# Kernel optimization log

Measured on AMD Instinct MI355X. Metric: run time of the kernel, lower is better.

## Reference

```python
import jax, jax.numpy as jnp
import numpy as np

N, E = 50000, 500000
IN_C, HID, OUT_C, HEADS, NL = 128, 16, 16, 8, 4
EPS = 1e-5
NEG_SLOPE = 0.2


def _gatv2(x, src, dst, Wl, Wr, att, bias, concat):
    # GATv2Conv (PyG semantics, eval mode): lin_l on source, lin_r on target,
    # e = a . LeakyReLU(xl[src] + xr[dst]); segment softmax over dst; scatter-sum.
    n = x.shape[0]
    H, C = att.shape
    xl = (x @ Wl).reshape(n, H, C)
    xr = (x @ Wr).reshape(n, H, C)
    e = jax.nn.leaky_relu(xl[src] + xr[dst], NEG_SLOPE)          # [E', H, C]
    logit = jnp.einsum('ehc,hc->eh', e, att)                      # [E', H]
    mx = jax.lax.stop_gradient(jax.ops.segment_max(logit, dst, num_segments=n))
    a = jnp.exp(logit - mx[dst])
    denom = jax.ops.segment_sum(a, dst, num_segments=n)
    alpha = a / denom[dst]                                        # [E', H]
    out = jax.ops.segment_sum(xl[src] * alpha[..., None], dst, num_segments=n)
    out = out.reshape(n, H * C) if concat else out.mean(axis=1)
    return out + bias


def _bn_eval(x, g, b, m, v):
    return (x - m) * jax.lax.rsqrt(v + EPS) * g + b


def setup_inputs() -> dict:
    key = jax.random.key(0)
    ks = jax.random.split(key, 32)
    d = {}
    d['x'] = jax.random.normal(ks[0], (N, IN_C), dtype=jnp.float32)
    d['edge_index'] = jax.random.randint(ks[1], (2, E), 0, N, dtype=jnp.int64)
    HC = HID * HEADS  # 128
    dims_in = [IN_C, HC, HC, HC]
    dims_h = [HEADS, HEADS, HEADS, 1]
    dims_c = [HID, HID, HID, OUT_C]
    ki = 2
    for i in range(NL):
        fan = dims_in[i]
        s = 1.0 / np.sqrt(fan)
        d[f'W{i}l'] = jax.random.uniform(ks[ki], (fan, dims_h[i] * dims_c[i]), minval=-s, maxval=s, dtype=jnp.float32); ki += 1
        d[f'W{i}r'] = jax.random.uniform(ks[ki], (fan, dims_h[i] * dims_c[i]), minval=-s, maxval=s, dtype=jnp.float32); ki += 1
        d[f'a{i}'] = jax.random.normal(ks[ki], (dims_h[i], dims_c[i]), dtype=jnp.float32) * 0.1; ki += 1
        out_dim = dims_h[i] * dims_c[i] if i < NL - 1 else dims_c[i]
        d[f'b{i}'] = jnp.zeros((out_dim,), dtype=jnp.float32)
    for i in range(NL - 1):
        d[f'g{i}'] = jnp.ones((HC,), dtype=jnp.float32) + 0.1 * jax.random.normal(ks[ki], (HC,), dtype=jnp.float32); ki += 1
        d[f'be{i}'] = 0.1 * jax.random.normal(ks[ki], (HC,), dtype=jnp.float32); ki += 1
        d[f'm{i}'] = 0.1 * jax.random.normal(ks[ki], (HC,), dtype=jnp.float32); ki += 1
        d[f'v{i}'] = jnp.ones((HC,), dtype=jnp.float32)
    return d


def reference(x, edge_index, W0l, W0r, a0, b0, W1l, W1r, a1, b1, W2l, W2r, a2, b2, W3l, W3r, a3, b3, g0, be0, m0, v0, g1, be1, m1, v1, g2, be2, m2, v2):
    n = x.shape[0]
    loop = jnp.arange(n, dtype=edge_index.dtype)
    src = jnp.concatenate([edge_index[0], loop])  # add_self_loops=True (PyG default)
    dst = jnp.concatenate([edge_index[1], loop])
    Ws = [(W0l, W0r, a0, b0), (W1l, W1r, a1, b1), (W2l, W2r, a2, b2), (W3l, W3r, a3, b3)]
    bns = [(g0, be0, m0, v0), (g1, be1, m1, v1), (g2, be2, m2, v2)]
    h = x
    for i in range(NL):
        Wl, Wr, att, bias = Ws[i]
        h = _gatv2(h, src, dst, Wl, Wr, att, bias, concat=(i < NL - 1))
        if i < NL - 1:
            g, b, m, v = bns[i]
            h = jax.nn.elu(_bn_eval(h, g, b, m, v))
    return h
```

## Files before the change

kernel.cpp:

```cpp
#include <hip/hip_runtime.h>
#include <hip/hip_fp16.h>
#include <math.h>

static constexpr float BN_EPS = 1e-5f;
static constexpr float NEG = 0.2f;

typedef float f32x4 __attribute__((ext_vector_type(4)));
typedef _Float16 h16x2 __attribute__((ext_vector_type(2)));
typedef _Float16 h16x8 __attribute__((ext_vector_type(8)));


__global__ void hist_kernel(const int* __restrict__ ei, int E, int n, int* __restrict__ cnt) {
    int e = blockIdx.x * blockDim.x + threadIdx.x;
    int ET = E + n;
    if (e >= ET) return;
    int d = (e < E) ? ei[E + e] : (e - E);
    atomicAdd(&cnt[d], 1);
}

__global__ void scan_block(const int* __restrict__ cnt, int* __restrict__ rowptr,
                           int* __restrict__ bsums, int n) {
    __shared__ int s[1024];
    int i = blockIdx.x * 1024 + threadIdx.x;
    int vv = (i < n) ? cnt[i] : 0;
    s[threadIdx.x] = vv;
    __syncthreads();
    for (int d = 1; d < 1024; d <<= 1) {
        int t = (threadIdx.x >= d) ? s[threadIdx.x - d] : 0;
        __syncthreads();
        s[threadIdx.x] += t;
        __syncthreads();
    }
    if (i < n) rowptr[i + 1] = s[threadIdx.x];
    if (threadIdx.x == 1023) bsums[blockIdx.x] = s[1023];
}

__global__ void scan_bsums(int* __restrict__ bsums, int nb) {
    int L = threadIdx.x;
    int v = (L < nb) ? bsums[L] : 0;
    for (int d = 1; d < 64; d <<= 1) {
        int t = __shfl_up(v, d);
        if (L >= d) v += t;
    }
    int ex = __shfl_up(v, 1);
    if (L == 0) ex = 0;
    if (L < nb) bsums[L] = ex;
}

__global__ void scan_add(int* __restrict__ rowptr, const int* __restrict__ bsums, int n) {
    int i = blockIdx.x * 1024 + threadIdx.x;
    if (i < n) rowptr[i + 1] += bsums[blockIdx.x];
    if (i == 0) rowptr[0] = 0;
}

__global__ void scatter_kernel(const int* __restrict__ ei, int E, int n,
                               const int* __restrict__ rowptr, int* __restrict__ fill,
                               int* __restrict__ col) {
    int e = blockIdx.x * blockDim.x + threadIdx.x;
    int ET = E + n;
    if (e >= ET) return;
    int s, d;
    if (e < E) { s = ei[e]; d = ei[E + e]; } else { s = e - E; d = s; }
    int pos = atomicAdd(&fill[d], 1);
    col[rowptr[d] + pos] = s;
}


__global__ void convert_h(const float* __restrict__ x, __half* __restrict__ xh, int total4) {
    int i = blockIdx.x * blockDim.x + threadIdx.x;
    if (i >= total4) return;
    float4 v = *(const float4*)&x[(size_t)i * 4];
    __half h[4] = {__float2half(v.x), __float2half(v.y), __float2half(v.z), __float2half(v.w)};
    *(ushort4*)&xh[(size_t)i * 4] = make_ushort4(
        __half_as_ushort(h[0]), __half_as_ushort(h[1]),
        __half_as_ushort(h[2]), __half_as_ushort(h[3]));
}


__global__ void pack_w(const float* __restrict__ Wl, const float* __restrict__ Wr,
                       __half* __restrict__ packed, int M, int NTT) {
    int tile = blockIdx.x;
    int NT = NTT >> 1;
    int gnt = tile % NTT;
    int kt = tile / NTT;
    int l = threadIdx.x;
    const float* W = (gnt < NT) ? Wl : Wr;
    int col = (gnt % NT) * 16 + (l & 15);
    int krow = kt * 32 + ((l >> 4) << 3);
    size_t base = (size_t)tile * 512 + (size_t)l * 8;
#pragma unroll
    for (int j = 0; j < 8; j++)
        packed[base + j] = __float2half(W[(size_t)(krow + j) * M + col]);
}


__global__ __launch_bounds__(256) void gemm_h_big(
    const __half* __restrict__ xh, const __half* __restrict__ packed,
    __half* __restrict__ Y1, __half* __restrict__ Y2, int n) {
    __shared__ _Float16 sA[64 * 136];
    const int t = threadIdx.x;
    const int row0 = blockIdx.x * 64;

    for (int c = t; c < 1024; c += 256) {
        int row = c >> 4;
        int off = (c & 15) * 8;
        int gr = row0 + row;
        if (gr >= n) gr = n - 1;
        *(h16x8*)&sA[row * 136 + off] = *(const h16x8*)&xh[(size_t)gr * 128 + off];
    }
    __syncthreads();

    const int lane = t & 63;
    const int s = t >> 6;
    const int lr = lane & 15;
    const int kq = (lane >> 4) * 8;

    h16x8 af[4][4];
#pragma unroll
    for (int rt = 0; rt < 4; rt++)
#pragma unroll
        for (int kt = 0; kt < 4; kt++)
            af[rt][kt] = *(const h16x8*)&sA[(rt * 16 + lr) * 136 + kt * 32 + kq];

    f32x4 acc[4][4];
#pragma unroll
    for (int a = 0; a < 4; a++)
#pragma unroll
        for (int b = 0; b < 4; b++) acc[a][b] = (f32x4){0.f, 0.f, 0.f, 0.f};

#pragma unroll
    for (int kt = 0; kt < 4; kt++) {
#pragma unroll
        for (int ntl = 0; ntl < 4; ntl++) {
            int nt = s * 4 + ntl;
            h16x8 b = *(const h16x8*)&packed[((size_t)(kt * 16 + nt)) * 512 + lane * 8];
#pragma unroll
            for (int rt = 0; rt < 4; rt++)
                acc[ntl][rt] = __builtin_amdgcn_mfma_f32_16x16x32_f16(af[rt][kt], b, acc[ntl][rt], 0, 0, 0);
        }
    }

    __half* Y = (s < 2) ? Y1 : Y2;
    const int colh = (s & 1) * 64;
    const int rq = (lane >> 4) * 4;
#pragma unroll
    for (int ntl = 0; ntl < 4; ntl++) {
        int col = colh + ntl * 16 + lr;
#pragma unroll
        for (int rt = 0; rt < 4; rt++) {
#pragma unroll
            for (int g = 0; g < 4; g++) {
                int row = row0 + rt * 16 + rq + g;
                if (row < n) Y[(size_t)row * 128 + col] = __float2half(acc[ntl][rt][g]);
            }
        }
    }
}


__global__ __launch_bounds__(256) void gemm_h_small(
    const __half* __restrict__ xh, const __half* __restrict__ packed,
    float* __restrict__ Y1, float* __restrict__ Y2, int n) {
    int lane = threadIdx.x & 63;
    int wv = blockIdx.x * 4 + (threadIdx.x >> 6);
    int row0 = wv * 16;
    if (row0 >= n) return;
    int r = row0 + (lane & 15);
    if (r >= n) r = n - 1;
    int kq = (lane >> 4) * 8;

    h16x8 af[4];
#pragma unroll
    for (int kt = 0; kt < 4; kt++)
        af[kt] = *(const h16x8*)&xh[(size_t)r * 128 + kt * 32 + kq];

    f32x4 acc[2];
    acc[0] = (f32x4){0.f, 0.f, 0.f, 0.f};
    acc[1] = (f32x4){0.f, 0.f, 0.f, 0.f};

#pragma unroll
    for (int kt = 0; kt < 4; kt++) {
#pragma unroll
        for (int nt = 0; nt < 2; nt++) {
            h16x8 b = *(const h16x8*)&packed[((size_t)(kt * 2 + nt)) * 512 + lane * 8];
            acc[nt] = __builtin_amdgcn_mfma_f32_16x16x32_f16(af[kt], b, acc[nt], 0, 0, 0);
        }
    }

    int colb = lane & 15;
    int rbase = row0 + (lane >> 4) * 4;
#pragma unroll
    for (int nt = 0; nt < 2; nt++) {
        float* Y = (nt == 0) ? Y1 : Y2;
#pragma unroll
        for (int g = 0; g < 4; g++) {
            int row = rbase + g;
            if (row < n) Y[(size_t)row * 16 + colb] = acc[nt][g];
        }
    }
}


__device__ __forceinline__ float dot4_h(h16x2 l01, h16x2 l23,
                                        h16x2 a01, h16x2 a23) {
#if __has_builtin(__builtin_amdgcn_fdot2)
    float part = __builtin_amdgcn_fdot2(l01, a01, 0.f, false);
    return __builtin_amdgcn_fdot2(l23, a23, part, false);
#else
    return fmaf((float)l01.x, (float)a01.x, fmaf((float)l01.y, (float)a01.y,
           fmaf((float)l23.x, (float)a23.x, (float)l23.y * (float)a23.y)));
#endif
}

__global__ __launch_bounds__(256) void agg_h(
    const __half* __restrict__ xl, const __half* __restrict__ xr,
    const int* __restrict__ rowptr, const int* __restrict__ col,
    const float* __restrict__ att, const float* __restrict__ bias,
    const float* __restrict__ g, const float* __restrict__ be,
    const float* __restrict__ bm, const float* __restrict__ bv,
    __half* __restrict__ oh, int n) {
    int v = (blockIdx.x * blockDim.x + threadIdx.x) >> 6;
    if (v >= n) return;
    int lane = threadIdx.x & 63;
    int half = lane >> 5;
    int L = lane & 31;
    int ch = 4 * L;

    float2 rraw = *(const float2*)&xr[(size_t)v * 128 + ch];
    h16x2 rx01 = *(h16x2*)&rraw.x;
    h16x2 rx23 = *(h16x2*)&rraw.y;
    float4 av = *(const float4*)&att[ch];
    h16x2 a01 = {(_Float16)av.x, (_Float16)av.y};
    h16x2 a23 = {(_Float16)av.z, (_Float16)av.w};
    const h16x2 neg2 = {(_Float16)NEG, (_Float16)NEG};

    int beg = rowptr[v];
    int end = rowptr[v + 1];

    float lrun = 0.f;
    float4 acc = make_float4(0.f, 0.f, 0.f, 0.f);

    auto proc = [&](float2 raw, bool ok) {
        h16x2 h01 = *(h16x2*)&raw.x;
        h16x2 h23 = *(h16x2*)&raw.y;
        h16x2 s01 = h01 + rx01;
        h16x2 s23 = h23 + rx23;
        h16x2 l01 = __builtin_elementwise_max(s01, s01 * neg2);
        h16x2 l23 = __builtin_elementwise_max(s23, s23 * neg2);
        float part = dot4_h(l01, l23, a01, a23);
        part += __shfl_xor(part, 1);
        part += __shfl_xor(part, 2);
        float p = ok ? __expf(part) : 0.f;
        lrun += p;
        acc.x = fmaf(p, (float)h01.x, acc.x);
        acc.y = fmaf(p, (float)h01.y, acc.y);
        acc.z = fmaf(p, (float)h23.x, acc.z);
        acc.w = fmaf(p, (float)h23.y, acc.w);
    };

    int e = beg;
    for (; e + 8 <= end; e += 8) {
        float2 r[4];
#pragma unroll
        for (int j = 0; j < 4; j++) {
            int u = col[e + 2 * j + half];
            r[j] = *(const float2*)&xl[((size_t)u << 7) + ch];
        }
#pragma unroll
        for (int j = 0; j < 4; j++) proc(r[j], true);
    }
    for (; e < end; e += 4) {
        float2 r[2];
        bool ok[2];
#pragma unroll
        for (int j = 0; j < 2; j++) {
            int idx = e + 2 * j + half;
            ok[j] = (idx < end);
            r[j] = make_float2(0.f, 0.f);
            if (ok[j]) {
                int u = col[idx];
                r[j] = *(const float2*)&xl[((size_t)u << 7) + ch];
            }
        }
#pragma unroll
        for (int j = 0; j < 2; j++) proc(r[j], ok[j]);
    }

    lrun += __shfl_xor(lrun, 32);
    acc.x += __shfl_xor(acc.x, 32);
    acc.y += __shfl_xor(acc.y, 32);
    acc.z += __shfl_xor(acc.z, 32);
    acc.w += __shfl_xor(acc.w, 32);

    if (half == 0) {
        float inv = 1.0f / lrun;
        float4 b4 = *(const float4*)&bias[ch];
        float o[4] = {fmaf(acc.x, inv, b4.x), fmaf(acc.y, inv, b4.y),
                      fmaf(acc.z, inv, b4.z), fmaf(acc.w, inv, b4.w)};
        float4 m4 = *(const float4*)&bm[ch];
        float4 v4 = *(const float4*)&bv[ch];
        float4 g4 = *(const float4*)&g[ch];
        float4 e4 = *(const float4*)&be[ch];
        float ms[4] = {m4.x, m4.y, m4.z, m4.w};
        float vs[4] = {v4.x, v4.y, v4.z, v4.w};
        float gs[4] = {g4.x, g4.y, g4.z, g4.w};
        float es[4] = {e4.x, e4.y, e4.z, e4.w};
        unsigned short h[4];
#pragma unroll
        for (int j = 0; j < 4; j++) {
            o[j] = (o[j] - ms[j]) * rsqrtf(vs[j] + BN_EPS) * gs[j] + es[j];
            o[j] = o[j] > 0.f ? o[j] : expm1f(o[j]);
            h[j] = __half_as_ushort(__float2half(o[j]));
        }
        *(ushort4*)&oh[(size_t)v * 128 + ch] = make_ushort4(h[0], h[1], h[2], h[3]);
    }
}


__global__ __launch_bounds__(256) void agg_f(
    const float* __restrict__ xl, const float* __restrict__ xr,
    const int* __restrict__ rowptr, const int* __restrict__ col,
    const float* __restrict__ att, const float* __restrict__ bias,
    float* __restrict__ out, int n) {
    int v = (blockIdx.x * blockDim.x + threadIdx.x) >> 6;
    if (v >= n) return;
    int lane = threadIdx.x & 63;
    int slot = lane >> 2;
    int L = lane & 3;
    int ch = 4 * L;

    float4 xrv = *(const float4*)&xr[(size_t)v * 16 + ch];
    float4 av = *(const float4*)&att[ch];
    int beg = rowptr[v];
    int end = rowptr[v + 1];

    float lrun = 0.f;
    float4 acc = make_float4(0.f, 0.f, 0.f, 0.f);

    for (int eb = beg; eb < end; eb += 16) {
        int idx = eb + slot;
        bool ok = (idx < end);
        float4 xv = make_float4(0.f, 0.f, 0.f, 0.f);
        if (ok) {
            int u = col[idx];
            xv = *(const float4*)&xl[((size_t)u << 4) + ch];
        }
        float s0 = xv.x + xrv.x; s0 = s0 > 0.f ? s0 : NEG * s0;
        float s1 = xv.y + xrv.y; s1 = s1 > 0.f ? s1 : NEG * s1;
        float s2 = xv.z + xrv.z; s2 = s2 > 0.f ? s2 : NEG * s2;
        float s3 = xv.w + xrv.w; s3 = s3 > 0.f ? s3 : NEG * s3;
        float part = fmaf(s0, av.x, fmaf(s1, av.y, fmaf(s2, av.z, s3 * av.w)));
        part += __shfl_xor(part, 1);
        part += __shfl_xor(part, 2);
        float p = ok ? __expf(part) : 0.f;
        lrun += p;
        acc.x = fmaf(p, xv.x, acc.x);
        acc.y = fmaf(p, xv.y, acc.y);
        acc.z = fmaf(p, xv.z, acc.z);
        acc.w = fmaf(p, xv.w, acc.w);
    }

#pragma unroll
    for (int d = 4; d < 64; d <<= 1) {
        lrun += __shfl_xor(lrun, d);
        acc.x += __shfl_xor(acc.x, d);
        acc.y += __shfl_xor(acc.y, d);
        acc.z += __shfl_xor(acc.z, d);
        acc.w += __shfl_xor(acc.w, d);
    }

    if (slot == 0) {
        float inv = 1.0f / lrun;
        float4 b4 = *(const float4*)&bias[ch];
        *(float4*)&out[(size_t)v * 16 + ch] =
            make_float4(fmaf(acc.x, inv, b4.x), fmaf(acc.y, inv, b4.y),
                        fmaf(acc.z, inv, b4.z), fmaf(acc.w, inv, b4.w));
    }
}


extern "C" void kernel_launch(void* const* d_in, const int* in_sizes, int n_in,
                              void* d_out, int out_size, void* d_ws, size_t ws_size,
                              hipStream_t stream) {
    const float* x = (const float*)d_in[0];
    const int* ei = (const int*)d_in[1];
    const float* Wl[4] = {(const float*)d_in[2], (const float*)d_in[6],
                          (const float*)d_in[10], (const float*)d_in[14]};
    const float* Wr[4] = {(const float*)d_in[3], (const float*)d_in[7],
                          (const float*)d_in[11], (const float*)d_in[15]};
    const float* att[4] = {(const float*)d_in[4], (const float*)d_in[8],
                           (const float*)d_in[12], (const float*)d_in[16]};
    const float* bias[4] = {(const float*)d_in[5], (const float*)d_in[9],
                            (const float*)d_in[13], (const float*)d_in[17]};
    const float* g[3] = {(const float*)d_in[18], (const float*)d_in[22], (const float*)d_in[26]};
    const float* be[3] = {(const float*)d_in[19], (const float*)d_in[23], (const float*)d_in[27]};
    const float* bm[3] = {(const float*)d_in[20], (const float*)d_in[24], (const float*)d_in[28]};
    const float* bv[3] = {(const float*)d_in[21], (const float*)d_in[25], (const float*)d_in[29]};

    const int n = in_sizes[0] / 128;
    const int E = in_sizes[1] / 2;
    const int ET = E + n;

    char* p = (char*)d_ws;
    __half* xh = (__half*)p;           p += (size_t)n * 128 * 2;
    __half* xlh = (__half*)p;          p += (size_t)n * 128 * 2;
    __half* xrh = (__half*)p;          p += (size_t)n * 128 * 2;
    float* xl3 = (float*)p;            p += (size_t)n * 16 * 4;
    float* xr3 = (float*)p;            p += (size_t)n * 16 * 4;
    int* rowptr = (int*)p;            p += (size_t)(n + 1) * 4;
    int* cnt = (int*)p;               p += (size_t)n * 4;
    int* fill = (int*)p;              p += (size_t)n * 4;
    int* col = (int*)p;               p += (size_t)ET * 4;
    int* bsums = (int*)p;             p += 256;
    __half* pk[4];
    for (int i = 0; i < 3; i++) { pk[i] = (__half*)p; p += 4 * 16 * 512 * 2; }
    pk[3] = (__half*)p;               p += 4 * 2 * 512 * 2;

    (void)hipMemsetAsync(cnt, 0, (size_t)n * 4, stream);
    (void)hipMemsetAsync(fill, 0, (size_t)n * 4, stream);

    const int tb = 256;
    hist_kernel<<<(ET + tb - 1) / tb, tb, 0, stream>>>(ei, E, n, cnt);
    int nb = (n + 1023) / 1024;
    scan_block<<<nb, 1024, 0, stream>>>(cnt, rowptr, bsums, n);
    scan_bsums<<<1, 64, 0, stream>>>(bsums, nb);
    scan_add<<<nb, 1024, 0, stream>>>(rowptr, bsums, n);
    scatter_kernel<<<(ET + tb - 1) / tb, tb, 0, stream>>>(ei, E, n, rowptr, fill, col);

    convert_h<<<(n * 32 + 255) / 256, 256, 0, stream>>>(x, xh, n * 32);
    for (int i = 0; i < 3; i++)
        pack_w<<<4 * 16, 64, 0, stream>>>(Wl[i], Wr[i], pk[i], 128, 16);
    pack_w<<<4 * 2, 64, 0, stream>>>(Wl[3], Wr[3], pk[3], 16, 2);

    const int gb64 = (n + 63) / 64;
    const int gemmBlocksSmall = ((n + 15) / 16 + 3) / 4;
    const int aggBlocks = (n + 3) / 4;

    for (int i = 0; i < 3; i++) {
        gemm_h_big<<<gb64, 256, 0, stream>>>(xh, pk[i], xlh, xrh, n);
        agg_h<<<aggBlocks, 256, 0, stream>>>(
            xlh, xrh, rowptr, col, att[i], bias[i], g[i], be[i], bm[i], bv[i],
            xh, n);
    }
    gemm_h_small<<<gemmBlocksSmall, 256, 0, stream>>>(xh, pk[3], xl3, xr3, n);
    agg_f<<<aggBlocks, 256, 0, stream>>>(
        xl3, xr3, rowptr, col, att[3], bias[3], (float*)d_out, n);
}
```

Measured before the change: 385.4 us.

## Process four edges per wavefront with 16-byte loads in fp16 aggregation

New measurement: 415.8 us. +7.9%, slower.

```diff
diff --git a/kernel.cpp b/kernel.cpp
--- a/kernel.cpp
+++ b/kernel.cpp
@@ -201,14 +201,11 @@
 }
 
 
-__device__ __forceinline__ float dot4_h(h16x2 l01, h16x2 l23,
-                                        h16x2 a01, h16x2 a23) {
+__device__ __forceinline__ float fdot2w(h16x2 x, h16x2 y, float init) {
 #if __has_builtin(__builtin_amdgcn_fdot2)
-    float part = __builtin_amdgcn_fdot2(l01, a01, 0.f, false);
-    return __builtin_amdgcn_fdot2(l23, a23, part, false);
+    return __builtin_amdgcn_fdot2(x, y, init, false);
 #else
-    return fmaf((float)l01.x, (float)a01.x, fmaf((float)l01.y, (float)a01.y,
-           fmaf((float)l23.x, (float)a23.x, (float)l23.y * (float)a23.y)));
+    return fmaf((float)x.x, (float)y.x, fmaf((float)x.y, (float)y.y, init));
 #endif
 }
 
@@ -222,97 +219,85 @@
     int v = (blockIdx.x * blockDim.x + threadIdx.x) >> 6;
     if (v >= n) return;
     int lane = threadIdx.x & 63;
-    int half = lane >> 5;
-    int L = lane & 31;
-    int ch = 4 * L;
-
-    float2 rraw = *(const float2*)&xr[(size_t)v * 128 + ch];
-    h16x2 rx01 = *(h16x2*)&rraw.x;
-    h16x2 rx23 = *(h16x2*)&rraw.y;
-    float4 av = *(const float4*)&att[ch];
-    h16x2 a01 = {(_Float16)av.x, (_Float16)av.y};
-    h16x2 a23 = {(_Float16)av.z, (_Float16)av.w};
-    const h16x2 neg2 = {(_Float16)NEG, (_Float16)NEG};
+    int slot = lane >> 4;
+    int L = lane & 15;
+    int ch = 8 * L;
+
+    h16x8 rx = *(const h16x8*)&xr[(size_t)v * 128 + ch];
+    h16x2 a01, a23, a45, a67;
+    {
+        float4 f0 = *(const float4*)&att[ch];
+        float4 f1 = *(const float4*)&att[ch + 4];
+        a01 = (h16x2){(_Float16)f0.x, (_Float16)f0.y};
+        a23 = (h16x2){(_Float16)f0.z, (_Float16)f0.w};
+        a45 = (h16x2){(_Float16)f1.x, (_Float16)f1.y};
+        a67 = (h16x2){(_Float16)f1.z, (_Float16)f1.w};
+    }
+    const h16x8 negv = {(_Float16)NEG, (_Float16)NEG, (_Float16)NEG, (_Float16)NEG,
+                        (_Float16)NEG, (_Float16)NEG, (_Float16)NEG, (_Float16)NEG};
 
     int beg = rowptr[v];
     int end = rowptr[v + 1];
 
     float lrun = 0.f;
-    float4 acc = make_float4(0.f, 0.f, 0.f, 0.f);
-
-    auto proc = [&](float2 raw, bool ok) {
-        h16x2 h01 = *(h16x2*)&raw.x;
-        h16x2 h23 = *(h16x2*)&raw.y;
-        h16x2 s01 = h01 + rx01;
-        h16x2 s23 = h23 + rx23;
-        h16x2 l01 = __builtin_elementwise_max(s01, s01 * neg2);
-        h16x2 l23 = __builtin_elementwise_max(s23, s23 * neg2);
-        float part = dot4_h(l01, l23, a01, a23);
+    float acc[8];
+#pragma unroll
+    for (int k = 0; k < 8; k++) acc[k] = 0.f;
+
+    for (int eb = beg; eb < end; eb += 4) {
+        int idx = eb + slot;
+        bool ok = (idx < end);
+        h16x8 x = (h16x8){0, 0, 0, 0, 0, 0, 0, 0};
+        if (ok) {
+            int u = col[idx];
+            x = *(const h16x8*)&xl[((size_t)u << 7) + ch];
+        }
+        h16x8 s = x + rx;
+        h16x8 l = __builtin_elementwise_max(s, s * negv);
+        float part = fdot2w((h16x2){l[0], l[1]}, a01, 0.f);
+        part = fdot2w((h16x2){l[2], l[3]}, a23, part);
+        part = fdot2w((h16x2){l[4], l[5]}, a45, part);
+        part = fdot2w((h16x2){l[6], l[7]}, a67, part);
         part += __shfl_xor(part, 1);
-        part += __shfl_xor(part, 2);
         float p = ok ? __expf(part) : 0.f;
         lrun += p;
-        acc.x = fmaf(p, (float)h01.x, acc.x);
-        acc.y = fmaf(p, (float)h01.y, acc.y);
-        acc.z = fmaf(p, (float)h23.x, acc.z);
-        acc.w = fmaf(p, (float)h23.y, acc.w);
-    };
-
-    int e = beg;
-    for (; e + 8 <= end; e += 8) {
-        float2 r[4];
-#pragma unroll
-        for (int j = 0; j < 4; j++) {
-            int u = col[e + 2 * j + half];
-            r[j] = *(const float2*)&xl[((size_t)u << 7) + ch];
-        }
-#pragma unroll
-        for (int j = 0; j < 4; j++) proc(r[j], true);
-    }
-    for (; e < end; e += 4) {
-        float2 r[2];
-        bool ok[2];
-#pragma unroll
-        for (int j = 0; j < 2; j++) {
-            int idx = e + 2 * j + half;
-            ok[j] = (idx < end);
-            r[j] = make_float2(0.f, 0.f);
-            if (ok[j]) {
-                int u = col[idx];
-                r[j] = *(const float2*)&xl[((size_t)u << 7) + ch];
+#pragma unroll
+        for (int k = 0; k < 8; k++) acc[k] = fmaf(p, (float)x[k], acc[k]);
+    }
+
+#pragma unroll
+    for (int d = 16; d < 64; d <<= 1) {
+        lrun += __shfl_xor(lrun, d);
+#pragma unroll
+        for (int k = 0; k < 8; k++) acc[k] += __shfl_xor(acc[k], d);
+    }
+
+    if (slot == 0) {
+        float inv = 1.0f / lrun;
+        unsigned short h[8];
+#pragma unroll
+        for (int q = 0; q < 2; q++) {
+            int c4 = ch + q * 4;
+            float4 b4 = *(const float4*)&bias[c4];
+            float4 m4 = *(const float4*)&bm[c4];
+            float4 v4 = *(const float4*)&bv[c4];
+            float4 g4 = *(const float4*)&g[c4];
+            float4 e4 = *(const float4*)&be[c4];
+            float bs[4] = {b4.x, b4.y, b4.z, b4.w};
+            float ms[4] = {m4.x, m4.y, m4.z, m4.w};
+            float vs[4] = {v4.x, v4.y, v4.z, v4.w};
+            float gs[4] = {g4.x, g4.y, g4.z, g4.w};
+            float es[4] = {e4.x, e4.y, e4.z, e4.w};
+#pragma unroll
+            for (int j = 0; j < 4; j++) {
+                float o = fmaf(acc[q * 4 + j], inv, bs[j]);
+                o = (o - ms[j]) * rsqrtf(vs[j] + BN_EPS) * gs[j] + es[j];
+                o = o > 0.f ? o : expm1f(o);
+                h[q * 4 + j] = __half_as_ushort(__float2half(o));
             }
         }
-#pragma unroll
-        for (int j = 0; j < 2; j++) proc(r[j], ok[j]);
-    }
-
-    lrun += __shfl_xor(lrun, 32);
-    acc.x += __shfl_xor(acc.x, 32);
-    acc.y += __shfl_xor(acc.y, 32);
-    acc.z += __shfl_xor(acc.z, 32);
-    acc.w += __shfl_xor(acc.w, 32);
-
-    if (half == 0) {
-        float inv = 1.0f / lrun;
-        float4 b4 = *(const float4*)&bias[ch];
-        float o[4] = {fmaf(acc.x, inv, b4.x), fmaf(acc.y, inv, b4.y),
-                      fmaf(acc.z, inv, b4.z), fmaf(acc.w, inv, b4.w)};
-        float4 m4 = *(const float4*)&bm[ch];
-        float4 v4 = *(const float4*)&bv[ch];
-        float4 g4 = *(const float4*)&g[ch];
-        float4 e4 = *(const float4*)&be[ch];
-        float ms[4] = {m4.x, m4.y, m4.z, m4.w};
-        float vs[4] = {v4.x, v4.y, v4.z, v4.w};
-        float gs[4] = {g4.x, g4.y, g4.z, g4.w};
-        float es[4] = {e4.x, e4.y, e4.z, e4.w};
-        unsigned short h[4];
-#pragma unroll
-        for (int j = 0; j < 4; j++) {
-            o[j] = (o[j] - ms[j]) * rsqrtf(vs[j] + BN_EPS) * gs[j] + es[j];
-            o[j] = o[j] > 0.f ? o[j] : expm1f(o[j]);
-            h[j] = __half_as_ushort(__float2half(o[j]));
-        }
         *(ushort4*)&oh[(size_t)v * 128 + ch] = make_ushort4(h[0], h[1], h[2], h[3]);
+        *(ushort4*)&oh[(size_t)v * 128 + ch + 4] = make_ushort4(h[4], h[5], h[6], h[7]);
     }
 }
 
```
